# Optimization experiments

Hardware: AMD Instinct MI355X
Metric: run time of the kernel (lower is better)

## Reference

```python
import jax, jax.numpy as jnp
import numpy as np

STRIDE = (1, 1)
PAD = (1, 1)

def setup_inputs() -> dict:
    key = jax.random.key(0)
    k1, k2, k3 = jax.random.split(key, 3)
    x = jax.random.normal(k1, (32, 128, 56, 56), dtype=jnp.float32)
    # K ~ N(0,1) per nn.init.normal_(self.K)
    K = jax.random.normal(k2, (256, 128, 3, 3), dtype=jnp.float32)
    bias = jax.random.normal(k3, (1,), dtype=jnp.float32)  # single scalar bias added to whole output
    return {"x": x, "K": K, "bias": bias}

def reference(x, K, bias):
    # Cross-correlation (torch conv semantics), NCHW / OIHW, zero padding.
    y = jax.lax.conv_general_dilated(
        x, K,
        window_strides=STRIDE,
        padding=[(PAD[0], PAD[0]), (PAD[1], PAD[1])],
        dimension_numbers=("NCHW", "OIHW", "NCHW"),
    )
    # Original adds a single scalar bias to the entire output tensor.
    return y + bias
```

## Files before the change

### kernel.cpp

```cpp
#include <hip/hip_runtime.h>

typedef __bf16 bf16x8 __attribute__((ext_vector_type(8)));
typedef float  floatx16 __attribute__((ext_vector_type(16)));

#define HW   56
#define NPIX 3136
#define CIN  128
#define COUT 256

#define AS_GLOBAL __attribute__((address_space(1)))
#define AS_LDS    __attribute__((address_space(3)))

__global__ __launch_bounds__(256) void wt_transform_kernel(
        const float* __restrict__ Kw, __bf16* __restrict__ W2) {
    int idx = blockIdx.x * 256 + threadIdx.x;
    int j     = idx & 7;
    int oc    = (idx >> 3) & 255;
    int cg    = (idx >> 11) & 3;
    int tapcc = idx >> 13;
    int tap   = tapcc % 9;
    int cc    = tapcc / 9;
    int c = cc * 32 + cg * 8 + j;
    W2[idx] = (__bf16)Kw[oc * 1152 + c * 9 + tap];
}

__device__ __forceinline__ int xs_idx(int row, int wp, int cg) {
    return row * 2640 + wp * 40 + cg * 8;
}

__global__ __launch_bounds__(512, 4) void conv_kernel(
        const float* __restrict__ x, const __bf16* __restrict__ W2,
        const float* __restrict__ bias, float* __restrict__ out) {
    __shared__ __align__(16) __bf16 Xs[6 * 2640];
    __shared__ __align__(16) __bf16 Abuf[3][4096];

    const int t    = threadIdx.x;
    const int nb   = blockIdx.x / 14;
    const int ht   = blockIdx.x % 14;
    const int h0   = ht * 4;
    const int ocb  = blockIdx.y * 128;

    const int wid  = t >> 6;
    const int lane = t & 63;
    const int half = lane >> 5;
    const int l31  = lane & 31;

    const int oc_rel = (wid & 1) * 64;
    const int prow   = wid >> 1;
    const int aocc   = (oc_rel + l31) * 8;

    floatx16 acc[2][2];
    #pragma unroll
    for (int mi = 0; mi < 2; ++mi)
        #pragma unroll
        for (int nj = 0; nj < 2; ++nj)
            #pragma unroll
            for (int k = 0; k < 16; ++k)
                acc[mi][nj][k] = 0.f;

    if (t < 240) {
        int cg   = t & 3;
        int rest = t >> 2;
        int row  = rest / 10;
        int zw   = rest % 10;
        int wp   = (zw == 0) ? 0 : (56 + zw);
        *(int4*)&Xs[xs_idx(row, wp, cg)] = make_int4(0, 0, 0, 0);
    }

    auto dma_a = [&](int cc, int tap, int b) {
        const __bf16* src = W2 + (size_t)(cc * 9 + tap) * 8192
                          + (t >> 7) * 2048 + (size_t)(ocb + (t & 127)) * 8;
        __builtin_amdgcn_global_load_lds(
            (const AS_GLOBAL unsigned*)(const void*)src,
            (AS_LDS unsigned*)(void*)&Abuf[b][t * 8], 16, 0, 0);
    };

    const int  sw     = t & 63;
    const int  sgr    = t >> 6;
    const int  sg     = sgr & 3;
    const int  rg2    = sgr >> 2;
    const bool wvalid = sw < 56;

    for (int cc = 0; cc < 4; ++cc) {
        __syncthreads();
        dma_a(cc, 0, 0);
        dma_a(cc, 1, 1);
        #pragma unroll
        for (int p = 0; p < 3; ++p) {
            int row = rg2 * 3 + p;
            int hin = h0 - 1 + row;
            bf16x8 v;
            #pragma unroll
            for (int j = 0; j < 8; ++j) v[j] = (__bf16)0.f;
            if (wvalid && (unsigned)hin < 56u) {
                const float* src = x + (size_t)(nb * CIN + cc * 32 + sg * 8) * NPIX
                                     + hin * HW + sw;
                #pragma unroll
                for (int j = 0; j < 8; ++j)
                    v[j] = (__bf16)src[j * NPIX];
            }
            if (wvalid)
                *(bf16x8*)&Xs[xs_idx(row, 1 + sw, sg)] = v;
        }
        __syncthreads();

        #pragma unroll
        for (int tap = 0; tap < 9; ++tap) {
            if (tap >= 2) {
                if (tap == 8) asm volatile("s_waitcnt vmcnt(0)" ::: "memory");
                else          asm volatile("s_waitcnt vmcnt(1)" ::: "memory");
            }
            if (tap >= 1) __builtin_amdgcn_s_barrier();
            if (tap < 7) dma_a(cc, tap + 2, (tap + 2) % 3);

            const int r = tap / 3, s = tap % 3;
            const __bf16* At = &Abuf[tap % 3][0];
            #pragma unroll
            for (int kc = 0; kc < 2; ++kc) {
                bf16x8 afr[2];
                #pragma unroll
                for (int mi = 0; mi < 2; ++mi)
                    afr[mi] = *(const bf16x8*)&At[(kc * 2 + half) * 1024 + aocc + mi * 256];
                bf16x8 bfr[2];
                #pragma unroll
                for (int nj = 0; nj < 2; ++nj) {
                    int pw = nj * 32 + l31;
                    bfr[nj] = *(const bf16x8*)&Xs[xs_idx(prow + r, pw + s, kc * 2 + half)];
                }
                #pragma unroll
                for (int mi = 0; mi < 2; ++mi)
                    #pragma unroll
                    for (int nj = 0; nj < 2; ++nj)
                        acc[mi][nj] = __builtin_amdgcn_mfma_f32_32x32x16_bf16(
                            afr[mi], bfr[nj], acc[mi][nj], 0, 0, 0);
            }
        }
    }

    const float bv = bias[0];
    const int hout = h0 + prow;
    const int oc_base = ocb + oc_rel;
    #pragma unroll
    for (int nj = 0; nj < 2; ++nj) {
        int pw = nj * 32 + l31;
        if (pw < 56) {
            #pragma unroll
            for (int mi = 0; mi < 2; ++mi) {
                #pragma unroll
                for (int rg = 0; rg < 16; ++rg) {
                    int oc = oc_base + mi * 32 + (rg & 3) + ((rg >> 2) << 3) + half * 4;
                    out[(size_t)(nb * COUT + oc) * NPIX + hout * HW + pw] = acc[mi][nj][rg] + bv;
                }
            }
        }
    }
}

extern "C" void kernel_launch(void* const* d_in, const int* in_sizes, int n_in,
                              void* d_out, int out_size, void* d_ws, size_t ws_size,
                              hipStream_t stream) {
    const float* x    = (const float*)d_in[0];
    const float* Kw   = (const float*)d_in[1];
    const float* bias = (const float*)d_in[2];
    float* out = (float*)d_out;
    __bf16* W2 = (__bf16*)d_ws;

    wt_transform_kernel<<<dim3(1152), dim3(256), 0, stream>>>(Kw, W2);
    conv_kernel<<<dim3(32 * 14, 2), dim3(512), 0, stream>>>(x, W2, bias, out);
}
```

Before: 190.2 us.

## Stage weight taps in groups of three with double-buffered prefetch

Restructures the weight-tile pipeline. It moves from a ring of three single-tap LDS buffers to two buffers that each hold three taps (one filter row). This cuts the barriers and wait points per channel chunk from about nine to three, and the next chunk's middle tap group is prefetched during the last group's compute. Wave priority is raised around the MFMA groups. LDS use per block grows by about 24KB, which risks occupancy, and a whole group's loads must land before it can be used, so latency hiding is coarser.

```diff
diff --git a/kernel.cpp b/kernel.cpp
--- a/kernel.cpp
+++ b/kernel.cpp
@@ -32,7 +32,7 @@
         const float* __restrict__ x, const __bf16* __restrict__ W2,
         const float* __restrict__ bias, float* __restrict__ out) {
     __shared__ __align__(16) __bf16 Xs[6 * 2640];
-    __shared__ __align__(16) __bf16 Abuf[3][4096];
+    __shared__ __align__(16) __bf16 Abuf[2][3 * 4096];
 
     const int t    = threadIdx.x;
     const int nb   = blockIdx.x / 14;
@@ -67,12 +67,39 @@
         *(int4*)&Xs[xs_idx(row, wp, cg)] = make_int4(0, 0, 0, 0);
     }
 
-    auto dma_a = [&](int cc, int tap, int b) {
+    auto dma_a = [&](int cc, int tap, int buf, int slot) {
         const __bf16* src = W2 + (size_t)(cc * 9 + tap) * 8192
                           + (t >> 7) * 2048 + (size_t)(ocb + (t & 127)) * 8;
         __builtin_amdgcn_global_load_lds(
             (const AS_GLOBAL unsigned*)(const void*)src,
-            (AS_LDS unsigned*)(void*)&Abuf[b][t * 8], 16, 0, 0);
+            (AS_LDS unsigned*)(void*)&Abuf[buf][slot * 4096 + t * 8], 16, 0, 0);
+    };
+
+    auto compute_group = [&](int g, int b) {
+        __builtin_amdgcn_s_setprio(1);
+        #pragma unroll
+        for (int tp = 0; tp < 3; ++tp) {
+            const __bf16* At = &Abuf[b][tp * 4096];
+            #pragma unroll
+            for (int kc = 0; kc < 2; ++kc) {
+                bf16x8 afr[2];
+                #pragma unroll
+                for (int mi = 0; mi < 2; ++mi)
+                    afr[mi] = *(const bf16x8*)&At[(kc * 2 + half) * 1024 + aocc + mi * 256];
+                bf16x8 bfr[2];
+                #pragma unroll
+                for (int nj = 0; nj < 2; ++nj)
+                    bfr[nj] = *(const bf16x8*)&Xs[xs_idx(prow + g, nj * 32 + l31 + tp,
+                                                         kc * 2 + half)];
+                #pragma unroll
+                for (int mi = 0; mi < 2; ++mi)
+                    #pragma unroll
+                    for (int nj = 0; nj < 2; ++nj)
+                        acc[mi][nj] = __builtin_amdgcn_mfma_f32_32x32x16_bf16(
+                            afr[mi], bfr[nj], acc[mi][nj], 0, 0, 0);
+            }
+        }
+        __builtin_amdgcn_s_setprio(0);
     };
 
     const int  sw     = t & 63;
@@ -83,8 +110,12 @@
 
     for (int cc = 0; cc < 4; ++cc) {
         __syncthreads();
-        dma_a(cc, 0, 0);
-        dma_a(cc, 1, 1);
+        #pragma unroll
+        for (int tp = 0; tp < 3; ++tp) dma_a(cc, tp, 0, tp);
+        if (cc == 0) {
+            #pragma unroll
+            for (int tp = 0; tp < 3; ++tp) dma_a(0, 3 + tp, 1, tp);
+        }
         #pragma unroll
         for (int p = 0; p < 3; ++p) {
             int row = rg2 * 3 + p;
@@ -104,37 +135,22 @@
         }
         __syncthreads();
 
+        compute_group(0, 0);
+
+        __builtin_amdgcn_s_barrier();
         #pragma unroll
-        for (int tap = 0; tap < 9; ++tap) {
-            if (tap >= 2) {
-                if (tap == 8) asm volatile("s_waitcnt vmcnt(0)" ::: "memory");
-                else          asm volatile("s_waitcnt vmcnt(1)" ::: "memory");
-            }
-            if (tap >= 1) __builtin_amdgcn_s_barrier();
-            if (tap < 7) dma_a(cc, tap + 2, (tap + 2) % 3);
+        for (int tp = 0; tp < 3; ++tp) dma_a(cc, 6 + tp, 0, tp);
 
-            const int r = tap / 3, s = tap % 3;
-            const __bf16* At = &Abuf[tap % 3][0];
+        compute_group(1, 1);
+
+        asm volatile("s_waitcnt vmcnt(0)" ::: "memory");
+        __builtin_amdgcn_s_barrier();
+        if (cc < 3) {
             #pragma unroll
-            for (int kc = 0; kc < 2; ++kc) {
-                bf16x8 afr[2];
-                #pragma unroll
-                for (int mi = 0; mi < 2; ++mi)
-                    afr[mi] = *(const bf16x8*)&At[(kc * 2 + half) * 1024 + aocc + mi * 256];
-                bf16x8 bfr[2];
-                #pragma unroll
-                for (int nj = 0; nj < 2; ++nj) {
-                    int pw = nj * 32 + l31;
-                    bfr[nj] = *(const bf16x8*)&Xs[xs_idx(prow + r, pw + s, kc * 2 + half)];
-                }
-                #pragma unroll
-                for (int mi = 0; mi < 2; ++mi)
-                    #pragma unroll
-                    for (int nj = 0; nj < 2; ++nj)
-                        acc[mi][nj] = __builtin_amdgcn_mfma_f32_32x32x16_bf16(
-                            afr[mi], bfr[nj], acc[mi][nj], 0, 0, 0);
-            }
+            for (int tp = 0; tp < 3; ++tp) dma_a(cc + 1, 3 + tp, 1, tp);
         }
+
+        compute_group(2, 0);
     }
 
     const float bv = bias[0];
```

After: 192.5 us. Within noise of the previous version (+1.2%).
